# Kernel optimization log

Measured on AMD Instinct MI355X. Metric: run time of the kernel, lower is better.

The kernel has to match this reference:

```python
import jax, jax.numpy as jnp
import numpy as np

D_MODEL, D_HEAD, N_HEAD = 1024, 64, 16
B, T1, T2 = 2, 2048, 2048


def setup_inputs() -> dict:
    key = jax.random.key(0)
    ks = jax.random.split(key, 8)
    s = 1.0 / np.sqrt(D_MODEL)
    return {
        "x": jax.random.normal(ks[0], (B, T1, D_MODEL), dtype=jnp.float32),
        "context": jax.random.normal(ks[1], (B, T2, D_MODEL), dtype=jnp.float32),
        "bias": jax.random.normal(ks[2], (T1, T2), dtype=jnp.float32),
        "W_q": jax.random.normal(ks[3], (D_MODEL, N_HEAD * D_HEAD), dtype=jnp.float32) * s,
        "W_k": jax.random.normal(ks[4], (D_MODEL, N_HEAD * D_HEAD), dtype=jnp.float32) * s,
        "W_v": jax.random.normal(ks[5], (D_MODEL, N_HEAD * D_HEAD), dtype=jnp.float32) * s,
        "W_out": jax.random.normal(ks[6], (N_HEAD * D_HEAD, D_MODEL), dtype=jnp.float32) * s,
        "b_out": jnp.zeros((D_MODEL,), dtype=jnp.float32),
    }


def reference(x, context, bias, W_q, W_k, W_v, W_out, b_out):
    Bq, T1_, _ = x.shape
    T2_ = context.shape[1]
    atten_scale = 1.0 / np.sqrt(D_HEAD)
    # fixed (non-trainable) per-head scale: 2^{-1}, ..., 2^{-n_head}
    head_scale = jnp.exp2(-jnp.arange(1, N_HEAD + 1, dtype=jnp.float32))

    # projections -> [B, H, T, d]
    q = (x @ W_q).reshape(Bq, T1_, N_HEAD, D_HEAD).transpose(0, 2, 1, 3)
    k = (context @ W_k).reshape(Bq, T2_, N_HEAD, D_HEAD).transpose(0, 2, 1, 3)
    v = (context @ W_v).reshape(Bq, T2_, N_HEAD, D_HEAD).transpose(0, 2, 1, 3)

    # scores: [B, H, T1, T2]
    scores = jnp.einsum("bhqd,bhkd->bhqk", q, k) * atten_scale
    scores = scores + bias[None, None, :, :] * head_scale[None, :, None, None]
    attn = jax.nn.softmax(scores, axis=-1)

    out = jnp.einsum("bhqk,bhkd->bqhd", attn, v).reshape(Bq, T1_, N_HEAD * D_HEAD)
    # dropout is identity in eval mode
    return out @ W_out + b_out
```

## Files before the change

kernel.cpp:

```cpp
#include <hip/hip_runtime.h>

typedef float  f32x4  __attribute__((ext_vector_type(4)));
typedef __bf16 bf16x8 __attribute__((ext_vector_type(8)));
typedef __bf16 bf16x4 __attribute__((ext_vector_type(4)));
typedef short  short8v __attribute__((ext_vector_type(8)));

__device__ __forceinline__ short f2bf(float f) {
  unsigned u = __float_as_uint(f);
  unsigned r = (u + 0x7FFFu + ((u >> 16) & 1u)) >> 16;
  return (short)r;
}

__device__ __forceinline__ f32x4 mfma16(bf16x8 a, bf16x8 b, f32x4 c) {
  return __builtin_amdgcn_mfma_f32_16x16x32_bf16(a, b, c, 0, 0, 0);
}

__device__ __forceinline__ void gload16(const void* g, void* l) {
  __builtin_amdgcn_global_load_lds(
      (const __attribute__((address_space(1))) unsigned int*)g,
      (__attribute__((address_space(3))) unsigned int*)l,
      16, 0, 0);
}


__global__ __launch_bounds__(256) void cvt_copy(const float* __restrict__ in,
                                                short* __restrict__ out, int n4) {
  int i = blockIdx.x * blockDim.x + threadIdx.x;
  int stride = gridDim.x * blockDim.x;
  for (; i < n4; i += stride) {
    float4 v = *(const float4*)&in[i * 4];
    short4 o;
    o.x = f2bf(v.x); o.y = f2bf(v.y); o.z = f2bf(v.z); o.w = f2bf(v.w);
    *(short4*)&out[i * 4] = o;
  }
}

__global__ __launch_bounds__(256) void cvt_transpose(const float* __restrict__ W,
                                                     short* __restrict__ Wt) {
  __shared__ short t_s[64][72];
  int k0 = blockIdx.y * 64, n0 = blockIdx.x * 64;
  int tid = threadIdx.x;
#pragma unroll
  for (int i = 0; i < 4; i++) {
    int idx = i * 256 + tid;
    int r = idx >> 4, cg = idx & 15;
    float4 v = *(const float4*)&W[(k0 + r) * 1024 + n0 + cg * 4];
    t_s[cg * 4 + 0][r] = f2bf(v.x);
    t_s[cg * 4 + 1][r] = f2bf(v.y);
    t_s[cg * 4 + 2][r] = f2bf(v.z);
    t_s[cg * 4 + 3][r] = f2bf(v.w);
  }
  __syncthreads();
#pragma unroll
  for (int i = 0; i < 2; i++) {
    int idx = i * 256 + tid;
    int r = idx >> 3, cg = idx & 7;
    short8v val = *(short8v*)&t_s[r][cg * 8];
    *(short8v*)&Wt[(n0 + r) * 1024 + k0 + cg * 8] = val;
  }
}

template <int EPI>
__global__ __launch_bounds__(256, 4) void gemm_bf16(const short* __restrict__ A,
                                                    const short* __restrict__ Bt,
                                                    void* __restrict__ out,
                                                    const float* __restrict__ bout) {
  constexpr int KD = 1024;
  __shared__ short a_s[64][64];
  __shared__ short b_s[64][64];
  int tid = threadIdx.x, w = tid >> 6, lane = tid & 63;
  int g = lane >> 4, c16 = lane & 15;
  int hsw = c16 & 7;

  int lin = blockIdx.x + 16 * blockIdx.y;
  int wk = (lin & 7) * 128 + (lin >> 3);
  int c0 = (wk & 15) * 64, r0 = (wk >> 4) * 64;

  int wr = (w >> 1) * 32, wc = (w & 1) * 32;
  f32x4 acc[2][2] = {};

  for (int kt = 0; kt < KD / 64; ++kt) {
    int k0 = kt * 64;
    __syncthreads();
#pragma unroll
    for (int i = 0; i < 2; i++) {
      int cb = i * 256 + w * 64;
      int c = cb + lane;
      int row = c >> 3, kg = c & 7;
      int sw = (kg ^ (row & 7)) * 8;
      gload16(A + (r0 + row) * KD + k0 + sw, (char*)a_s + cb * 16);
      gload16(Bt + (c0 + row) * KD + k0 + sw, (char*)b_s + cb * 16);
    }
    __syncthreads();
#pragma unroll
    for (int kk = 0; kk < 2; kk++) {
      bf16x8 af[2], bf[2];
      int sl0 = ((4 * kk + g) ^ hsw) * 8;
#pragma unroll
      for (int m = 0; m < 2; m++) af[m] = *(const bf16x8*)&a_s[wr + m * 16 + c16][sl0];
#pragma unroll
      for (int n = 0; n < 2; n++) bf[n] = *(const bf16x8*)&b_s[wc + n * 16 + c16][sl0];
#pragma unroll
      for (int m = 0; m < 2; m++)
#pragma unroll
        for (int n = 0; n < 2; n++) acc[m][n] = mfma16(af[m], bf[n], acc[m][n]);
    }
  }

#pragma unroll
  for (int m = 0; m < 2; m++)
#pragma unroll
    for (int n = 0; n < 2; n++)
#pragma unroll
      for (int r = 0; r < 4; r++) {
        int row = r0 + wr + m * 16 + g * 4 + r;
        int col = c0 + wc + n * 16 + c16;
        float v = acc[m][n][r];
        if (EPI == 2) {
          ((float*)out)[row * 1024 + col] = v + bout[col];
        } else {
          int b = row >> 11, t = row & 2047, h = col >> 6, d = col & 63;
          short bv = f2bf(v);
          if (EPI == 0)
            ((short*)out)[(((b * 16 + h) * 2048) + t) * 64 + d] = bv;
          else
            ((short*)out)[(((b * 16 + h) * 64) + d) * 2048 + t] = bv;
        }
      }
}

__global__ __launch_bounds__(512, 4) void flash_attn(const short* __restrict__ Qg,
                                                     const short* __restrict__ Kg,
                                                     const short* __restrict__ Vtg,
                                                     const float* __restrict__ bias,
                                                     short* __restrict__ Og) {
  __shared__ short k_s[2][64][64];
  __shared__ short v_s[2][64][64];
  __shared__ short p_s[8][16][64];

  int tid = threadIdx.x, w = tid >> 6, lane = tid & 63;
  int g = lane >> 4, c16 = lane & 15;

  int lin = blockIdx.x + 16 * (blockIdx.y + 16 * blockIdx.z);
  int wk = (lin & 7) * 64 + (lin >> 3);
  int qb = (wk & 15) * 128;
  int h = (wk >> 4) & 15;
  int b = wk >> 8;

  const short* Qh = Qg + (size_t)(b * 16 + h) * 2048 * 64;
  const short* Kh = Kg + (size_t)(b * 16 + h) * 2048 * 64;
  const short* Vh = Vtg + (size_t)(b * 16 + h) * 64 * 2048;

  const float C1 = 0.125f * 1.44269504f;
  const float C2 = exp2f(-(float)(h + 1)) * 1.44269504f;

  int qrow = qb + w * 16 + c16;
  const float* bp = bias + (size_t)qrow * 2048 + 4 * g;

  {
    int row = tid >> 3, t8 = tid & 7, sw = (t8 ^ (row & 7)) * 8;
    gload16(Kh + row * 64 + sw, (char*)&k_s[0][0][0] + (w * 64) * 16);
    gload16(Vh + row * 2048 + sw, (char*)&v_s[0][0][0] + (w * 64) * 16);
  }
  bf16x8 qreg0 = *(const bf16x8*)(Qh + (size_t)qrow * 64 + g * 8);
  bf16x8 qreg1 = *(const bf16x8*)(Qh + (size_t)qrow * 64 + 32 + g * 8);
  asm volatile("" ::: "memory");

  float l_run = 0.f;
  f32x4 o_acc[4] = {};
  const int hsw = c16 & 7;
  const int s0 = g ^ hsw;

  for (int kt = 0; kt < 32; ++kt) {
    int cur = kt & 1;
    float4 bv0 = *(const float4*)(bp + 0);
    float4 bv1 = *(const float4*)(bp + 16);
    float4 bv2 = *(const float4*)(bp + 32);
    float4 bv3 = *(const float4*)(bp + 48);
    bp += 64;

    if (kt < 31) {
      const short* Ks = Kh + (size_t)(kt + 1) * 64 * 64;
      const short* Vs = Vh + (kt + 1) * 64;
      int row = tid >> 3, t8 = tid & 7, sw = (t8 ^ (row & 7)) * 8;
      gload16(Ks + row * 64 + sw, (char*)&k_s[cur ^ 1][0][0] + (w * 64) * 16);
      gload16(Vs + row * 2048 + sw, (char*)&v_s[cur ^ 1][0][0] + (w * 64) * 16);
      asm volatile("s_waitcnt vmcnt(6)" ::: "memory");
    } else {
      asm volatile("s_waitcnt vmcnt(4)" ::: "memory");
    }
    __builtin_amdgcn_s_barrier();

    f32x4 sacc[4] = {};
    __builtin_amdgcn_s_setprio(1);
#pragma unroll
    for (int t = 0; t < 4; t++) {
      const short* kr = &k_s[cur][t * 16 + c16][0];
      bf16x8 kf0 = *(const bf16x8*)(kr + s0 * 8);
      bf16x8 kf1 = *(const bf16x8*)(kr + (s0 ^ 4) * 8);
      sacc[t] = mfma16(kf0, qreg0, sacc[t]);
      sacc[t] = mfma16(kf1, qreg1, sacc[t]);
    }
    __builtin_amdgcn_s_setprio(0);

    float lp = 0.f;
#pragma unroll
    for (int t = 0; t < 4; t++) {
      float4 bv = (t == 0) ? bv0 : (t == 1) ? bv1 : (t == 2) ? bv2 : bv3;
      float p0 = exp2f(sacc[t][0] * C1 + bv.x * C2);
      float p1 = exp2f(sacc[t][1] * C1 + bv.y * C2);
      float p2 = exp2f(sacc[t][2] * C1 + bv.z * C2);
      float p3 = exp2f(sacc[t][3] * C1 + bv.w * C2);
      lp += (p0 + p1) + (p2 + p3);
      bf16x4 pk = {(__bf16)p0, (__bf16)p1, (__bf16)p2, (__bf16)p3};
      int sl = (2 * t + (g >> 1)) ^ hsw;
      *(bf16x4*)&p_s[w][c16][sl * 8 + (g & 1) * 4] = pk;
    }
    l_run += lp;

    __builtin_amdgcn_s_setprio(1);
#pragma unroll
    for (int kk = 0; kk < 2; kk++) {
      int sp = (4 * kk + g) ^ hsw;
      bf16x8 pa = *(const bf16x8*)&p_s[w][c16][sp * 8];
#pragma unroll
      for (int dt = 0; dt < 4; dt++) {
        bf16x8 vb = *(const bf16x8*)&v_s[cur][dt * 16 + c16][sp * 8];
        o_acc[dt] = mfma16(pa, vb, o_acc[dt]);
      }
    }
    __builtin_amdgcn_s_setprio(0);
    __builtin_amdgcn_s_barrier();
  }

  l_run += __shfl_xor(l_run, 16);
  l_run += __shfl_xor(l_run, 32);
  float inv[4];
#pragma unroll
  for (int r = 0; r < 4; r++) inv[r] = 1.f / __shfl(l_run, 4 * g + r);

#pragma unroll
  for (int dt = 0; dt < 4; dt++)
#pragma unroll
    for (int r = 0; r < 4; r++) {
      int t = qb + w * 16 + 4 * g + r;
      Og[(size_t)(b * 2048 + t) * 1024 + h * 64 + dt * 16 + c16] =
          f2bf(o_acc[dt][r] * inv[r]);
    }
}

extern "C" void kernel_launch(void* const* d_in, const int* in_sizes, int n_in,
                              void* d_out, int out_size, void* d_ws, size_t ws_size,
                              hipStream_t stream) {
  const float* x    = (const float*)d_in[0];
  const float* ctx  = (const float*)d_in[1];
  const float* bias = (const float*)d_in[2];
  const float* Wq   = (const float*)d_in[3];
  const float* Wk   = (const float*)d_in[4];
  const float* Wv   = (const float*)d_in[5];
  const float* Wo   = (const float*)d_in[6];
  const float* bo   = (const float*)d_in[7];
  float* out = (float*)d_out;

  char* ws = (char*)d_ws;
  short* x_bf = (short*)(ws + 0);
  short* c_bf = (short*)(ws + 8388608);
  short* wq_t = (short*)(ws + 16777216);
  short* wk_t = (short*)(ws + 18874368);
  short* wv_t = (short*)(ws + 20971520);
  short* wo_t = (short*)(ws + 23068672);
  short* q_ws = (short*)(ws + 25165824);
  short* k_ws = (short*)(ws + 33554432);
  short* v_ws = (short*)(ws + 41943040);
  short* o_ws = (short*)(ws + 50331648);

  cvt_copy<<<1024, 256, 0, stream>>>(x, x_bf, 1048576);
  cvt_copy<<<1024, 256, 0, stream>>>(ctx, c_bf, 1048576);
  dim3 tg(16, 16);
  cvt_transpose<<<tg, 256, 0, stream>>>(Wq, wq_t);
  cvt_transpose<<<tg, 256, 0, stream>>>(Wk, wk_t);
  cvt_transpose<<<tg, 256, 0, stream>>>(Wv, wv_t);
  cvt_transpose<<<tg, 256, 0, stream>>>(Wo, wo_t);

  dim3 gg(16, 64);
  gemm_bf16<0><<<gg, 256, 0, stream>>>(x_bf, wq_t, q_ws, nullptr);
  gemm_bf16<0><<<gg, 256, 0, stream>>>(c_bf, wk_t, k_ws, nullptr);
  gemm_bf16<1><<<gg, 256, 0, stream>>>(c_bf, wv_t, v_ws, nullptr);

  dim3 fg(16, 16, 2);
  flash_attn<<<fg, 512, 0, stream>>>(q_ws, k_ws, v_ws, bias, o_ws);

  gemm_bf16<2><<<gg, 256, 0, stream>>>(o_ws, wo_t, out, bo);
}
```

Baseline: 160.3 us.

## Switch attention to 32x32 MFMA with register-resident P, fuse K/V projections

```diff
diff --git a/kernel.cpp b/kernel.cpp
--- a/kernel.cpp
+++ b/kernel.cpp
@@ -1,9 +1,11 @@
 #include <hip/hip_runtime.h>
 
-typedef float  f32x4  __attribute__((ext_vector_type(4)));
-typedef __bf16 bf16x8 __attribute__((ext_vector_type(8)));
-typedef __bf16 bf16x4 __attribute__((ext_vector_type(4)));
+typedef float  f32x4   __attribute__((ext_vector_type(4)));
+typedef float  f32x16  __attribute__((ext_vector_type(16)));
+typedef __bf16 bf16x8  __attribute__((ext_vector_type(8)));
+typedef __bf16 bf16x2  __attribute__((ext_vector_type(2)));
 typedef short  short8v __attribute__((ext_vector_type(8)));
+typedef unsigned uint4v __attribute__((ext_vector_type(4)));
 
 __device__ __forceinline__ short f2bf(float f) {
   unsigned u = __float_as_uint(f);
@@ -13,6 +15,9 @@
 
 __device__ __forceinline__ f32x4 mfma16(bf16x8 a, bf16x8 b, f32x4 c) {
   return __builtin_amdgcn_mfma_f32_16x16x32_bf16(a, b, c, 0, 0, 0);
+}
+__device__ __forceinline__ f32x16 mfma32(bf16x8 a, bf16x8 b, f32x16 c) {
+  return __builtin_amdgcn_mfma_f32_32x32x16_bf16(a, b, c, 0, 0, 0);
 }
 
 __device__ __forceinline__ void gload16(const void* g, void* l) {
@@ -35,9 +40,18 @@
   }
 }
 
-__global__ __launch_bounds__(256) void cvt_transpose(const float* __restrict__ W,
-                                                     short* __restrict__ Wt) {
+__global__ __launch_bounds__(256) void cvt_transpose4(const float* __restrict__ W0,
+                                                      const float* __restrict__ W1,
+                                                      const float* __restrict__ W2,
+                                                      const float* __restrict__ W3,
+                                                      short* __restrict__ T0,
+                                                      short* __restrict__ T1,
+                                                      short* __restrict__ T2,
+                                                      short* __restrict__ T3) {
   __shared__ short t_s[64][72];
+  int z = blockIdx.z;
+  const float* W = (z == 0) ? W0 : (z == 1) ? W1 : (z == 2) ? W2 : W3;
+  short* Wt = (z == 0) ? T0 : (z == 1) ? T1 : (z == 2) ? T2 : T3;
   int k0 = blockIdx.y * 64, n0 = blockIdx.x * 64;
   int tid = threadIdx.x;
 #pragma unroll
@@ -64,17 +78,19 @@
 __global__ __launch_bounds__(256, 4) void gemm_bf16(const short* __restrict__ A,
                                                     const short* __restrict__ Bt,
                                                     void* __restrict__ out,
+                                                    void* __restrict__ out2,
                                                     const float* __restrict__ bout) {
   constexpr int KD = 1024;
+  constexpr int NB = (EPI == 3) ? 32 : 16;
   __shared__ short a_s[64][64];
   __shared__ short b_s[64][64];
   int tid = threadIdx.x, w = tid >> 6, lane = tid & 63;
   int g = lane >> 4, c16 = lane & 15;
   int hsw = c16 & 7;
 
-  int lin = blockIdx.x + 16 * blockIdx.y;
-  int wk = (lin & 7) * 128 + (lin >> 3);
-  int c0 = (wk & 15) * 64, r0 = (wk >> 4) * 64;
+  int lin = blockIdx.x + NB * blockIdx.y;
+  int wk = (lin & 7) * (NB * 8) + (lin >> 3);
+  int c0 = (wk & (NB - 1)) * 64, r0 = (wk / NB) * 64;
 
   int wr = (w >> 1) * 32, wc = (w & 1) * 32;
   f32x4 acc[2][2] = {};
@@ -116,30 +132,36 @@
         int row = r0 + wr + m * 16 + g * 4 + r;
         int col = c0 + wc + n * 16 + c16;
         float v = acc[m][n][r];
+        int b = row >> 11, t = row & 2047;
         if (EPI == 2) {
           ((float*)out)[row * 1024 + col] = v + bout[col];
+        } else if (EPI == 0) {
+          int h = col >> 6, d = col & 63;
+          ((short*)out)[(((b * 16 + h) * 2048) + t) * 64 + d] = f2bf(v);
         } else {
-          int b = row >> 11, t = row & 2047, h = col >> 6, d = col & 63;
-          short bv = f2bf(v);
-          if (EPI == 0)
-            ((short*)out)[(((b * 16 + h) * 2048) + t) * 64 + d] = bv;
-          else
-            ((short*)out)[(((b * 16 + h) * 64) + d) * 2048 + t] = bv;
+          if (col < 1024) {
+            int h = col >> 6, d = col & 63;
+            ((short*)out)[(((b * 16 + h) * 2048) + t) * 64 + d] = f2bf(v);
+          } else {
+            int cv = col - 1024;
+            int h = cv >> 6, d = cv & 63;
+            ((short*)out2)[(((b * 16 + h) * 64) + d) * 2048 + t] = f2bf(v);
+          }
         }
       }
 }
 
-__global__ __launch_bounds__(512, 4) void flash_attn(const short* __restrict__ Qg,
+__global__ __launch_bounds__(256, 4) void flash_attn(const short* __restrict__ Qg,
                                                      const short* __restrict__ Kg,
                                                      const short* __restrict__ Vtg,
                                                      const float* __restrict__ bias,
                                                      short* __restrict__ Og) {
   __shared__ short k_s[2][64][64];
   __shared__ short v_s[2][64][64];
-  __shared__ short p_s[8][16][64];
 
   int tid = threadIdx.x, w = tid >> 6, lane = tid & 63;
-  int g = lane >> 4, c16 = lane & 15;
+  int hi = lane >> 5, ll = lane & 31;
+  int l7 = ll & 7;
 
   int lin = blockIdx.x + 16 * (blockIdx.y + 16 * blockIdx.z);
   int wk = (lin & 7) * 64 + (lin >> 3);
@@ -154,99 +176,119 @@
   const float C1 = 0.125f * 1.44269504f;
   const float C2 = exp2f(-(float)(h + 1)) * 1.44269504f;
 
-  int qrow = qb + w * 16 + c16;
-  const float* bp = bias + (size_t)qrow * 2048 + 4 * g;
-
-  {
-    int row = tid >> 3, t8 = tid & 7, sw = (t8 ^ (row & 7)) * 8;
-    gload16(Kh + row * 64 + sw, (char*)&k_s[0][0][0] + (w * 64) * 16);
-    gload16(Vh + row * 2048 + sw, (char*)&v_s[0][0][0] + (w * 64) * 16);
-  }
-  bf16x8 qreg0 = *(const bf16x8*)(Qh + (size_t)qrow * 64 + g * 8);
-  bf16x8 qreg1 = *(const bf16x8*)(Qh + (size_t)qrow * 64 + 32 + g * 8);
+  int qrow = qb + w * 32 + ll;
+  const float* bp = bias + (size_t)qrow * 2048 + 4 * hi;
+
+#pragma unroll
+  for (int i = 0; i < 2; i++) {
+    int cb = i * 256 + w * 64;
+    int c = cb + lane;
+    int row = c >> 3, t8 = c & 7, sw = (t8 ^ (row & 7)) * 8;
+    gload16(Kh + row * 64 + sw, (char*)&k_s[0][0][0] + cb * 16);
+    gload16(Vh + row * 2048 + sw, (char*)&v_s[0][0][0] + cb * 16);
+  }
+  bf16x8 qf[4];
+#pragma unroll
+  for (int dm = 0; dm < 4; dm++)
+    qf[dm] = *(const bf16x8*)(Qh + (size_t)qrow * 64 + dm * 16 + hi * 8);
   asm volatile("" ::: "memory");
 
   float l_run = 0.f;
-  f32x4 o_acc[4] = {};
-  const int hsw = c16 & 7;
-  const int s0 = g ^ hsw;
-
+  f32x16 o_acc[2] = {};
+
+#pragma unroll 2
   for (int kt = 0; kt < 32; ++kt) {
     int cur = kt & 1;
-    float4 bv0 = *(const float4*)(bp + 0);
-    float4 bv1 = *(const float4*)(bp + 16);
-    float4 bv2 = *(const float4*)(bp + 32);
-    float4 bv3 = *(const float4*)(bp + 48);
-    bp += 64;
+    f32x4 bv[2][4];
+#pragma unroll
+    for (int t = 0; t < 2; t++)
+#pragma unroll
+      for (int u = 0; u < 4; u++)
+        bv[t][u] = *(const f32x4*)(bp + kt * 64 + t * 32 + u * 8);
 
     if (kt < 31) {
       const short* Ks = Kh + (size_t)(kt + 1) * 64 * 64;
       const short* Vs = Vh + (kt + 1) * 64;
-      int row = tid >> 3, t8 = tid & 7, sw = (t8 ^ (row & 7)) * 8;
-      gload16(Ks + row * 64 + sw, (char*)&k_s[cur ^ 1][0][0] + (w * 64) * 16);
-      gload16(Vs + row * 2048 + sw, (char*)&v_s[cur ^ 1][0][0] + (w * 64) * 16);
-      asm volatile("s_waitcnt vmcnt(6)" ::: "memory");
+#pragma unroll
+      for (int i = 0; i < 2; i++) {
+        int cb = i * 256 + w * 64;
+        int c = cb + lane;
+        int row = c >> 3, t8 = c & 7, sw = (t8 ^ (row & 7)) * 8;
+        gload16(Ks + row * 64 + sw, (char*)&k_s[cur ^ 1][0][0] + cb * 16);
+        gload16(Vs + row * 2048 + sw, (char*)&v_s[cur ^ 1][0][0] + cb * 16);
+      }
+      asm volatile("s_waitcnt vmcnt(12)" ::: "memory");
     } else {
-      asm volatile("s_waitcnt vmcnt(4)" ::: "memory");
+      asm volatile("s_waitcnt vmcnt(8)" ::: "memory");
     }
     __builtin_amdgcn_s_barrier();
 
-    f32x4 sacc[4] = {};
+    f32x16 sacc[2] = {};
     __builtin_amdgcn_s_setprio(1);
 #pragma unroll
-    for (int t = 0; t < 4; t++) {
-      const short* kr = &k_s[cur][t * 16 + c16][0];
-      bf16x8 kf0 = *(const bf16x8*)(kr + s0 * 8);
-      bf16x8 kf1 = *(const bf16x8*)(kr + (s0 ^ 4) * 8);
-      sacc[t] = mfma16(kf0, qreg0, sacc[t]);
-      sacc[t] = mfma16(kf1, qreg1, sacc[t]);
-    }
+    for (int t = 0; t < 2; t++)
+#pragma unroll
+      for (int dm = 0; dm < 4; dm++) {
+        const short* kr = &k_s[cur][t * 32 + ll][((2 * dm + hi) ^ l7) * 8];
+        sacc[t] = mfma32(*(const bf16x8*)kr, qf[dm], sacc[t]);
+      }
     __builtin_amdgcn_s_setprio(0);
 
     float lp = 0.f;
-#pragma unroll
-    for (int t = 0; t < 4; t++) {
-      float4 bv = (t == 0) ? bv0 : (t == 1) ? bv1 : (t == 2) ? bv2 : bv3;
-      float p0 = exp2f(sacc[t][0] * C1 + bv.x * C2);
-      float p1 = exp2f(sacc[t][1] * C1 + bv.y * C2);
-      float p2 = exp2f(sacc[t][2] * C1 + bv.z * C2);
-      float p3 = exp2f(sacc[t][3] * C1 + bv.w * C2);
-      lp += (p0 + p1) + (p2 + p3);
-      bf16x4 pk = {(__bf16)p0, (__bf16)p1, (__bf16)p2, (__bf16)p3};
-      int sl = (2 * t + (g >> 1)) ^ hsw;
-      *(bf16x4*)&p_s[w][c16][sl * 8 + (g & 1) * 4] = pk;
+    bf16x8 PA[4];
+#pragma unroll
+    for (int t = 0; t < 2; t++) {
+      unsigned pk[8];
+#pragma unroll
+      for (int i = 0; i < 8; i++) {
+        float p0 = exp2f(sacc[t][2 * i] * C1 + bv[t][i >> 1][2 * (i & 1)] * C2);
+        float p1 = exp2f(sacc[t][2 * i + 1] * C1 + bv[t][i >> 1][2 * (i & 1) + 1] * C2);
+        lp += p0 + p1;
+        bf16x2 pp = {(__bf16)p0, (__bf16)p1};
+        pk[i] = __builtin_bit_cast(unsigned, pp);
+      }
+#pragma unroll
+      for (int a = 0; a < 2; a++) {
+        unsigned y1 = hi ? pk[4 * a + 0] : pk[4 * a + 2];
+        unsigned z1 = __shfl_xor(y1, 32);
+        unsigned y2 = hi ? pk[4 * a + 1] : pk[4 * a + 3];
+        unsigned z2 = __shfl_xor(y2, 32);
+        unsigned w0 = hi ? z1 : pk[4 * a + 0];
+        unsigned w1 = hi ? z2 : pk[4 * a + 1];
+        unsigned w2 = hi ? pk[4 * a + 2] : z1;
+        unsigned w3 = hi ? pk[4 * a + 3] : z2;
+        uint4v q4 = {w0, w1, w2, w3};
+        PA[2 * t + a] = __builtin_bit_cast(bf16x8, q4);
+      }
     }
     l_run += lp;
 
     __builtin_amdgcn_s_setprio(1);
 #pragma unroll
-    for (int kk = 0; kk < 2; kk++) {
-      int sp = (4 * kk + g) ^ hsw;
-      bf16x8 pa = *(const bf16x8*)&p_s[w][c16][sp * 8];
-#pragma unroll
-      for (int dt = 0; dt < 4; dt++) {
-        bf16x8 vb = *(const bf16x8*)&v_s[cur][dt * 16 + c16][sp * 8];
-        o_acc[dt] = mfma16(pa, vb, o_acc[dt]);
-      }
-    }
+    for (int dt = 0; dt < 2; dt++)
+#pragma unroll
+      for (int m = 0; m < 4; m++) {
+        const short* vr = &v_s[cur][dt * 32 + ll][((2 * m + hi) ^ l7) * 8];
+        o_acc[dt] = mfma32(PA[m], *(const bf16x8*)vr, o_acc[dt]);
+      }
     __builtin_amdgcn_s_setprio(0);
     __builtin_amdgcn_s_barrier();
   }
 
-  l_run += __shfl_xor(l_run, 16);
   l_run += __shfl_xor(l_run, 32);
-  float inv[4];
-#pragma unroll
-  for (int r = 0; r < 4; r++) inv[r] = 1.f / __shfl(l_run, 4 * g + r);
-
-#pragma unroll
-  for (int dt = 0; dt < 4; dt++)
-#pragma unroll
-    for (int r = 0; r < 4; r++) {
-      int t = qb + w * 16 + 4 * g + r;
-      Og[(size_t)(b * 2048 + t) * 1024 + h * 64 + dt * 16 + c16] =
-          f2bf(o_acc[dt][r] * inv[r]);
-    }
+  float invl = 1.f / l_run;
+
+#pragma unroll
+  for (int r = 0; r < 16; r++) {
+    int q = (r & 3) + 8 * (r >> 2) + 4 * hi;
+    float iv = __shfl(invl, q);
+    int tg = qb + w * 32 + q;
+#pragma unroll
+    for (int dt = 0; dt < 2; dt++) {
+      Og[(size_t)(b * 2048 + tg) * 1024 + h * 64 + dt * 32 + ll] =
+          f2bf(o_acc[dt][r] * iv);
+    }
+  }
 }
 
 extern "C" void kernel_launch(void* const* d_in, const int* in_sizes, int n_in,
@@ -276,19 +318,16 @@
 
   cvt_copy<<<1024, 256, 0, stream>>>(x, x_bf, 1048576);
   cvt_copy<<<1024, 256, 0, stream>>>(ctx, c_bf, 1048576);
-  dim3 tg(16, 16);
-  cvt_transpose<<<tg, 256, 0, stream>>>(Wq, wq_t);
-  cvt_transpose<<<tg, 256, 0, stream>>>(Wk, wk_t);
-  cvt_transpose<<<tg, 256, 0, stream>>>(Wv, wv_t);
-  cvt_transpose<<<tg, 256, 0, stream>>>(Wo, wo_t);
-
-  dim3 gg(16, 64);
-  gemm_bf16<0><<<gg, 256, 0, stream>>>(x_bf, wq_t, q_ws, nullptr);
-  gemm_bf16<0><<<gg, 256, 0, stream>>>(c_bf, wk_t, k_ws, nullptr);
-  gemm_bf16<1><<<gg, 256, 0, stream>>>(c_bf, wv_t, v_ws, nullptr);
+  dim3 tg(16, 16, 4);
+  cvt_transpose4<<<tg, 256, 0, stream>>>(Wq, Wk, Wv, Wo, wq_t, wk_t, wv_t, wo_t);
+
+  dim3 gq(16, 64);
+  gemm_bf16<0><<<gq, 256, 0, stream>>>(x_bf, wq_t, q_ws, nullptr, nullptr);
+  dim3 gkv(32, 64);
+  gemm_bf16<3><<<gkv, 256, 0, stream>>>(c_bf, wk_t, k_ws, v_ws, nullptr);
 
   dim3 fg(16, 16, 2);
-  flash_attn<<<fg, 512, 0, stream>>>(q_ws, k_ws, v_ws, bias, o_ws);
-
-  gemm_bf16<2><<<gg, 256, 0, stream>>>(o_ws, wo_t, out, bo);
-}
+  flash_attn<<<fg, 256, 0, stream>>>(q_ws, k_ws, v_ws, bias, o_ws);
+
+  gemm_bf16<2><<<gq, 256, 0, stream>>>(o_ws, wo_t, out, nullptr, bo);
+}
```

New measurement: 265.2 us. +65.4%, slower.
